# Kernel optimization log

Measured on AMD Instinct MI355X. Metric: run time of the kernel, lower is better.

The kernel has to match this reference:

```python
import jax, jax.numpy as jnp
import numpy as np
import math

B, L, DP, DB, H, DH = 1, 256, 128, 128, 8, 32


def _ln(x, g, b, eps=1e-5):
    m = x.mean(-1, keepdims=True)
    v = x.var(-1, keepdims=True)
    return (x - m) / jnp.sqrt(v + eps) * g + b


def setup_inputs() -> dict:
    key = jax.random.key(0)
    ks = jax.random.split(key, 12)
    s_in = 1.0 / math.sqrt(DP)
    s_hd = 1.0 / math.sqrt(H * DH)
    return {
        "pair": jax.random.normal(ks[0], (B, L, L, DP), jnp.float32),
        "bias": jax.random.normal(ks[1], (B, L, L, DB), jnp.float32),
        "mask": jax.random.randint(ks[2], (B, L), 0, 2, jnp.int32),
        "g_pair": jnp.ones((DP,), jnp.float32),
        "b_pair": jnp.zeros((DP,), jnp.float32),
        "g_bias": jnp.ones((DB,), jnp.float32),
        "b_bias": jnp.zeros((DB,), jnp.float32),
        "Wq": jax.random.normal(ks[3], (DP, H * DH), jnp.float32) * s_in,
        "Wk": jax.random.normal(ks[4], (DP, H * DH), jnp.float32) * s_in,
        "Wv": jax.random.normal(ks[5], (DP, H * DH), jnp.float32) * s_in,
        "Wb": jax.random.normal(ks[6], (DB, H), jnp.float32) * s_in,
        "Wg": jax.random.normal(ks[7], (DP, H * DH), jnp.float32) * s_in,
        "bg": jnp.ones((H * DH,), jnp.float32),
        "Wo": jax.random.normal(ks[8], (H * DH, DP), jnp.float32) * s_hd,
        "bo": jnp.zeros((DP,), jnp.float32),
    }


def reference(pair, bias, mask, g_pair, b_pair, g_bias, b_bias,
              Wq, Wk, Wv, Wb, Wg, bg, Wo, bo):
    is_row = True
    scaling = 1.0 / math.sqrt(DH)

    mask_b = (mask == 0)                               # [B,L], True = masked
    mask_2d = mask_b[:, None, :] | mask_b[:, :, None]  # [B,L,L]

    p = jnp.nan_to_num(pair)
    bi = jnp.nan_to_num(bias)
    if is_row:
        p = p.transpose(0, 2, 1, 3)
        bi = bi.transpose(0, 2, 1, 3)
        mask_2d = mask_2d.transpose(0, 2, 1)

    pn = _ln(p, g_pair, b_pair)        # [B,L,L,DP]
    bn = _ln(bi, g_bias, b_bias)       # [B,L,L,DB]

    q = (pn @ Wq).reshape(B, L, L, H, DH) * scaling
    k = (pn @ Wk).reshape(B, L, L, H, DH) / math.sqrt(L)
    v = (pn @ Wv).reshape(B, L, L, H, DH)
    b_proj = bn @ Wb                   # [B,L,L,H]
    gate = jax.nn.sigmoid(pn @ Wg + bg)  # [B,L,L,H*DH]

    # scores summed over the axial (n) axis AND head dim k
    attn = jnp.einsum('bnihk,bnjhk->bijh', q, k) + b_proj
    attn = jnp.where(mask_2d[..., None], -1e9, attn)
    attn = jax.nn.softmax(attn, axis=-2)  # over j

    out = jnp.einsum('bijh,bkjhd->bikhd', attn, v).reshape(B, L, L, H * DH)
    out = gate * out
    out = out @ Wo + bo                # [B,L,L,DP]
    if is_row:
        out = out.transpose(0, 2, 1, 3)
    # note: faithful to source — output mask uses the (permuted) mask_2d frame
    out = jnp.where(mask_2d[..., None], 0.0, out)
    return out
```

## Files before the change

### kernel.cpp

```cpp
#include <hip/hip_runtime.h>
#include <math.h>


typedef unsigned short u16;
typedef __attribute__((ext_vector_type(8))) short short8;
typedef __attribute__((ext_vector_type(4))) float float4v;

__device__ __forceinline__ u16 f2bf(float f) {
  unsigned int u = __float_as_uint(f);
  u += 0x7FFFu + ((u >> 16) & 1u);
  return (u16)(u >> 16);
}
__device__ __forceinline__ float bf2f(u16 h) {
  return __uint_as_float(((unsigned int)h) << 16);
}

__global__ __launch_bounds__(256) void k_ln(const float* __restrict__ x,
                                            const float* __restrict__ g,
                                            const float* __restrict__ b,
                                            u16* __restrict__ y) {
  int p = blockIdx.x * 4 + (threadIdx.x >> 6);
  int lane = threadIdx.x & 63;
  float2 xv = *(const float2*)(x + (size_t)p * 128 + lane * 2);
  float x0 = xv.x, x1 = xv.y;
  float s = x0 + x1, ss = x0 * x0 + x1 * x1;
#pragma unroll
  for (int off = 32; off; off >>= 1) {
    s += __shfl_xor(s, off);
    ss += __shfl_xor(ss, off);
  }
  float m = s * (1.0f / 128.0f);
  float v = ss * (1.0f / 128.0f) - m * m;
  float inv = rsqrtf(v + 1e-5f);
  float2 gv = *(const float2*)(g + lane * 2);
  float2 bv = *(const float2*)(b + lane * 2);
  float y0 = (x0 - m) * inv * gv.x + bv.x;
  float y1 = (x1 - m) * inv * gv.y + bv.y;
  unsigned int pk = (unsigned int)f2bf(y0) | ((unsigned int)f2bf(y1) << 16);
  *(unsigned int*)(y + (size_t)p * 128 + lane * 2) = pk;
}

__global__ __launch_bounds__(256) void k_lnbias_bproj(const float* __restrict__ x,
                                                      const float* __restrict__ g,
                                                      const float* __restrict__ b,
                                                      const float* __restrict__ Wb,
                                                      float* __restrict__ Bp) {
  const int t = threadIdx.x;
  const int row = t >> 3, h = t & 7;
  const int p = blockIdx.x * 32 + row;
  const int r = p >> 8, sc = p & 255;
  const float* rp = x + (size_t)p * 128 + h * 16;
  float4 xv[4];
#pragma unroll
  for (int i = 0; i < 4; ++i) xv[i] = ((const float4*)rp)[i];
  float s = 0.f, ss = 0.f;
#pragma unroll
  for (int i = 0; i < 4; ++i) {
    s += (xv[i].x + xv[i].y) + (xv[i].z + xv[i].w);
    ss += (xv[i].x * xv[i].x + xv[i].y * xv[i].y) + (xv[i].z * xv[i].z + xv[i].w * xv[i].w);
  }
#pragma unroll
  for (int off = 1; off <= 4; off <<= 1) {
    s += __shfl_xor(s, off);
    ss += __shfl_xor(ss, off);
  }
  float m = s * (1.0f / 128.0f);
  float var = ss * (1.0f / 128.0f) - m * m;
  float inv = rsqrtf(var + 1e-5f);
  float part[8];
#pragma unroll
  for (int hh = 0; hh < 8; ++hh) part[hh] = 0.f;
  const float4* g4 = (const float4*)(g + h * 16);
  const float4* b4 = (const float4*)(b + h * 16);
#pragma unroll
  for (int i4 = 0; i4 < 4; ++i4) {
    float4 gv = g4[i4], bv = b4[i4];
    float xs[4] = {xv[i4].x, xv[i4].y, xv[i4].z, xv[i4].w};
    float gs[4] = {gv.x, gv.y, gv.z, gv.w};
    float bs[4] = {bv.x, bv.y, bv.z, bv.w};
#pragma unroll
    for (int q = 0; q < 4; ++q) {
      int k = h * 16 + i4 * 4 + q;
      float xn = (xs[q] - m) * inv * gs[q] + bs[q];
      float4 w0 = *(const float4*)(Wb + k * 8);
      float4 w1 = *(const float4*)(Wb + k * 8 + 4);
      part[0] += xn * w0.x;
      part[1] += xn * w0.y;
      part[2] += xn * w0.z;
      part[3] += xn * w0.w;
      part[4] += xn * w1.x;
      part[5] += xn * w1.y;
      part[6] += xn * w1.z;
      part[7] += xn * w1.w;
    }
  }
#pragma unroll
  for (int off = 1; off <= 4; off <<= 1) {
#pragma unroll
    for (int hh = 0; hh < 8; ++hh) part[hh] += __shfl_xor(part[hh], off);
  }
  float val = (h == 0) ? part[0]
            : (h == 1) ? part[1]
            : (h == 2) ? part[2]
            : (h == 3) ? part[3]
            : (h == 4) ? part[4]
            : (h == 5) ? part[5]
            : (h == 6) ? part[6]
                       : part[7];
  Bp[(size_t)h * 65536 + (size_t)sc * 256 + r] = val;
}

__global__ __launch_bounds__(256) void k_wcvt(const float* __restrict__ Wq,
                                              const float* __restrict__ Wk,
                                              const float* __restrict__ Wv,
                                              const float* __restrict__ Wg,
                                              const float* __restrict__ Wo,
                                              u16* __restrict__ Wtb,
                                              u16* __restrict__ Wotb) {
  int idx = blockIdx.x * 256 + threadIdx.x;
  if (idx < 131072) {
    int w = idx >> 15, r = idx & 32767;
    int n = r >> 7, k = r & 127;
    const float* W = (w == 0) ? Wq : (w == 1) ? Wk : (w == 2) ? Wv : Wg;
    Wtb[(size_t)w * 32768 + n * 128 + k] = f2bf(W[k * 256 + n]);
  } else {
    int r = idx - 131072;
    int c = r >> 8, e = r & 255;
    Wotb[c * 256 + e] = f2bf(Wo[e * 128 + c]);
  }
}

__global__ __launch_bounds__(256) void k_proj_qkg(const u16* __restrict__ PNb,
                                                  const u16* __restrict__ Wtb,
                                                  const float* __restrict__ bg,
                                                  u16* __restrict__ Qr,
                                                  u16* __restrict__ Kr,
                                                  u16* __restrict__ Gb) {
  __shared__ u16 sb[128 * 72];
  const int t = threadIdx.x;
  const int wid = t >> 6, lane = t & 63;
  const int mrow = lane & 15, quad = lane >> 4;
  const int stripe = blockIdx.x;
  const int n0 = blockIdx.y * 64;
  const int wsel3 = blockIdx.z;
  const int wsel = (wsel3 == 2) ? 3 : wsel3;
  const u16* Wt = Wtb + (size_t)wsel * 32768;

  short8 bfr[4][4];
#pragma unroll
  for (int nt = 0; nt < 4; ++nt)
#pragma unroll
    for (int kk = 0; kk < 4; ++kk)
      bfr[nt][kk] = *(const short8*)(Wt + (size_t)(n0 + nt * 16 + mrow) * 128 + kk * 32 + quad * 8);

  float bgv[4];
#pragma unroll
  for (int nt = 0; nt < 4; ++nt) bgv[nt] = bg[n0 + nt * 16 + mrow];

  for (int it = 0; it < 4; ++it) {
    const int pb = stripe * 512 + it * 128;
    const int pw = pb + wid * 32;
    short8 afr[2][4];
#pragma unroll
    for (int mt = 0; mt < 2; ++mt)
#pragma unroll
      for (int kk = 0; kk < 4; ++kk)
        afr[mt][kk] =
            *(const short8*)(PNb + (size_t)(pw + mt * 16 + mrow) * 128 + kk * 32 + quad * 8);
    float4v acc[2][4];
#pragma unroll
    for (int mt = 0; mt < 2; ++mt)
#pragma unroll
      for (int nt = 0; nt < 4; ++nt) acc[mt][nt] = (float4v){0.f, 0.f, 0.f, 0.f};
#pragma unroll
    for (int kk = 0; kk < 4; ++kk)
#pragma unroll
      for (int mt = 0; mt < 2; ++mt)
#pragma unroll
        for (int nt = 0; nt < 4; ++nt)
          acc[mt][nt] = __builtin_amdgcn_mfma_f32_16x16x32_bf16(afr[mt][kk], bfr[nt][kk],
                                                                acc[mt][nt], 0, 0, 0);
#pragma unroll
    for (int mt = 0; mt < 2; ++mt)
#pragma unroll
      for (int nt = 0; nt < 4; ++nt)
#pragma unroll
        for (int reg = 0; reg < 4; ++reg) {
          float v = acc[mt][nt][reg];
          if (wsel3 == 0) v *= 0.17677669529663687f;
          else if (wsel3 == 1) v *= 0.0625f;
          else v = 1.f / (1.f + expf(-(v + bgv[nt])));
          sb[(wid * 32 + mt * 16 + quad * 4 + reg) * 72 + nt * 16 + mrow] = f2bf(v);
        }
    __syncthreads();
#pragma unroll
    for (int u4 = 0; u4 < 4; ++u4) {
      int u = u4 * 256 + t;
      int row = u >> 3, c8 = (u & 7) * 8;
      short8 vv = *(const short8*)&sb[row * 72 + c8];
      int p = pb + row;
      if (wsel3 == 0) {
        *(short8*)(Qr + (size_t)p * 256 + n0 + c8) = vv;
      } else if (wsel3 == 1) {
        *(short8*)(Kr + (size_t)p * 256 + n0 + c8) = vv;
      } else {
        int r = p >> 8, sc = p & 255;
        *(short8*)(Gb + ((size_t)sc * 256 + r) * 256 + n0 + c8) = vv;
      }
    }
    __syncthreads();
  }
}

__global__ __launch_bounds__(256) void k_projv(const u16* __restrict__ PNb,
                                               const u16* __restrict__ Wtb,
                                               u16* __restrict__ Vtb) {
  __shared__ u16 sb[128 * 136];
  const int t = threadIdx.x;
  const int wid = t >> 6, lane = t & 63;
  const int mrow = lane & 15, quad = lane >> 4;
  const int sc = blockIdx.x >> 1;
  const int r0 = (blockIdx.x & 1) * 128;
  short8 afr[2][4];
#pragma unroll
  for (int mt = 0; mt < 2; ++mt) {
    const int p = (r0 + wid * 32 + mt * 16 + mrow) * 256 + sc;
    const u16* ar = PNb + (size_t)p * 128 + quad * 8;
#pragma unroll
    for (int kk = 0; kk < 4; ++kk) afr[mt][kk] = *(const short8*)(ar + kk * 32);
  }
  const u16* Wt = Wtb + (size_t)2 * 32768;
  for (int half = 0; half < 2; ++half) {
#pragma unroll
    for (int nt8 = 0; nt8 < 8; ++nt8) {
      const int nt = half * 8 + nt8;
      float4v acc[2];
      acc[0] = (float4v){0.f, 0.f, 0.f, 0.f};
      acc[1] = (float4v){0.f, 0.f, 0.f, 0.f};
      const u16* br = Wt + (size_t)(nt * 16 + mrow) * 128 + quad * 8;
#pragma unroll
      for (int kk = 0; kk < 4; ++kk) {
        short8 bfr = *(const short8*)(br + kk * 32);
#pragma unroll
        for (int mt = 0; mt < 2; ++mt)
          acc[mt] = __builtin_amdgcn_mfma_f32_16x16x32_bf16(afr[mt][kk], bfr, acc[mt], 0, 0, 0);
      }
#pragma unroll
      for (int mt = 0; mt < 2; ++mt)
#pragma unroll
        for (int reg = 0; reg < 4; ++reg)
          sb[(wid * 32 + mt * 16 + quad * 4 + reg) * 136 + nt8 * 16 + mrow] =
              f2bf(acc[mt][reg]);
    }
    __syncthreads();
#pragma unroll
    for (int it = 0; it < 8; ++it) {
      int u = it * 256 + t;
      int c = u & 127, rg = u >> 7;
      short8 vv;
#pragma unroll
      for (int q = 0; q < 8; ++q) vv[q] = (short)sb[(rg * 8 + q) * 136 + c];
      int n = half * 128 + c;
      int h = n >> 5, d = n & 31;
      *(short8*)(Vtb + (size_t)h * 2097152 + (size_t)(sc * 32 + d) * 256 + r0 + rg * 8) = vv;
    }
    __syncthreads();
  }
}

__global__ __launch_bounds__(256) void k_logits_mfma(const u16* __restrict__ Qr,
                                                     const u16* __restrict__ Kr,
                                                     float* __restrict__ Lg2) {
  __shared__ u16 Qs[128 * 40];
  __shared__ u16 Ks[128 * 40];
  const int t = threadIdx.x;
  const int wid = t >> 6, lane = t & 63;
  const int mrow = lane & 15, quad = lane >> 4;
  const int i0 = (blockIdx.x >> 1) * 128, j0 = (blockIdx.x & 1) * 128;
  const int h = blockIdx.y;
  const int wi = wid >> 1, wj = wid & 1;
  float4v acc[4][4];
#pragma unroll
  for (int a = 0; a < 4; ++a)
#pragma unroll
    for (int bq = 0; bq < 4; ++bq) acc[a][bq] = (float4v){0.f, 0.f, 0.f, 0.f};

  for (int ck = 0; ck < 32; ++ck) {
    const int sc = blockIdx.z * 32 + ck;
    __syncthreads();
#pragma unroll
    for (int u = 0; u < 2; ++u) {
      int id = u * 256 + t;
      int rr = id >> 2, c8 = (id & 3) * 8;
      *(short8*)&Qs[rr * 40 + c8] =
          *(const short8*)(Qr + ((size_t)((i0 + rr) * 256 + sc)) * 256 + h * 32 + c8);
      *(short8*)&Ks[rr * 40 + c8] =
          *(const short8*)(Kr + ((size_t)((j0 + rr) * 256 + sc)) * 256 + h * 32 + c8);
    }
    __syncthreads();
    short8 afr[4], bfr[4];
#pragma unroll
    for (int mt = 0; mt < 4; ++mt)
      afr[mt] = *(const short8*)&Qs[(wi * 64 + mt * 16 + mrow) * 40 + quad * 8];
#pragma unroll
    for (int nn = 0; nn < 4; ++nn)
      bfr[nn] = *(const short8*)&Ks[(wj * 64 + nn * 16 + mrow) * 40 + quad * 8];
#pragma unroll
    for (int mt = 0; mt < 4; ++mt)
#pragma unroll
      for (int nn = 0; nn < 4; ++nn)
        acc[mt][nn] = __builtin_amdgcn_mfma_f32_16x16x32_bf16(afr[mt], bfr[nn], acc[mt][nn], 0, 0, 0);
  }
  float* slab = Lg2 + ((size_t)blockIdx.z * 8 + h) * 65536;
#pragma unroll
  for (int mt = 0; mt < 4; ++mt)
#pragma unroll
    for (int nn = 0; nn < 4; ++nn) {
      int j = j0 + wj * 64 + nn * 16 + mrow;
#pragma unroll
      for (int reg = 0; reg < 4; ++reg) {
        int i = i0 + wi * 64 + mt * 16 + quad * 4 + reg;
        slab[(size_t)i * 256 + j] = acc[mt][nn][reg];
      }
    }
}

__global__ __launch_bounds__(256) void k_softmax(const float* __restrict__ Bp,
                                                 const float* __restrict__ Lg2,
                                                 const int* __restrict__ mask,
                                                 u16* __restrict__ Ab) {
  const int i = blockIdx.x, h = blockIdx.y;
  const int j = threadIdx.x;
  __shared__ float red[4], red2[4];
  const size_t off = (size_t)h * 65536 + (size_t)i * 256 + j;
  float x = Bp[off];
#pragma unroll
  for (int z = 0; z < 8; ++z) x += Lg2[(size_t)z * 524288 + off];
  bool mi = (mask[i] == 0);
  if (mi || (mask[j] == 0)) x = -1e9f;
  float mx = x;
#pragma unroll
  for (int off2 = 32; off2; off2 >>= 1) mx = fmaxf(mx, __shfl_xor(mx, off2));
  int wave = j >> 6;
  if ((j & 63) == 0) red[wave] = mx;
  __syncthreads();
  mx = fmaxf(fmaxf(red[0], red[1]), fmaxf(red[2], red[3]));
  float e = expf(x - mx);
  float sm = e;
#pragma unroll
  for (int off2 = 32; off2; off2 >>= 1) sm += __shfl_xor(sm, off2);
  if ((j & 63) == 0) red2[wave] = sm;
  __syncthreads();
  sm = red2[0] + red2[1] + red2[2] + red2[3];
  Ab[off] = f2bf(e / sm);
}

__global__ __launch_bounds__(256) void k_av_mfma(const u16* __restrict__ Ab,
                                                 const u16* __restrict__ Vtb,
                                                 const u16* __restrict__ Gb,
                                                 u16* __restrict__ GOb) {
  __shared__ u16 As[64 * 264];
  const int t = threadIdx.x;
  const int wid = t >> 6, lane = t & 63;
  const int mrow = lane & 15, quad = lane >> 4;
  const int h = blockIdx.z;
  const int i0 = blockIdx.y * 64;
  const u16* ag = Ab + (size_t)h * 65536 + (size_t)i0 * 256;
#pragma unroll
  for (int u = 0; u < 8; ++u) {
    int id = u * 256 + t;
    int rr = id >> 5, c8 = (id & 31) * 8;
    *(short8*)&As[rr * 264 + c8] = *(const short8*)(ag + (size_t)rr * 256 + c8);
  }
  __syncthreads();
  const u16* vg = Vtb + (size_t)h * 2097152;
  for (int nt4 = 0; nt4 < 4; ++nt4) {
    const int nbase = blockIdx.x * 1024 + wid * 256 + nt4 * 64;
    float4v acc[4][4];
#pragma unroll
    for (int a = 0; a < 4; ++a)
#pragma unroll
      for (int bq = 0; bq < 4; ++bq) acc[a][bq] = (float4v){0.f, 0.f, 0.f, 0.f};
#pragma unroll
    for (int kk = 0; kk < 8; ++kk) {
      short8 afr[4], bfr[4];
#pragma unroll
      for (int mt = 0; mt < 4; ++mt)
        afr[mt] = *(const short8*)&As[(mt * 16 + mrow) * 264 + kk * 32 + quad * 8];
#pragma unroll
      for (int nn = 0; nn < 4; ++nn)
        bfr[nn] = *(const short8*)(vg + (size_t)(nbase + nn * 16 + mrow) * 256 + kk * 32 + quad * 8);
#pragma unroll
      for (int mt = 0; mt < 4; ++mt)
#pragma unroll
        for (int nn = 0; nn < 4; ++nn)
          acc[mt][nn] = __builtin_amdgcn_mfma_f32_16x16x32_bf16(afr[mt], bfr[nn], acc[mt][nn], 0, 0, 0);
    }
#pragma unroll
    for (int mt = 0; mt < 4; ++mt)
#pragma unroll
      for (int nn = 0; nn < 4; ++nn) {
        int n = nbase + nn * 16 + mrow;
        int kslot = n >> 5, d = n & 31;
        int e = h * 32 + d;
#pragma unroll
        for (int reg = 0; reg < 4; ++reg) {
          int i = i0 + mt * 16 + quad * 4 + reg;
          size_t idx = ((size_t)i * 256 + kslot) * 256 + e;
          float gv = bf2f(Gb[idx]);
          GOb[idx] = f2bf(acc[mt][nn][reg] * gv);
        }
      }
  }
}

__global__ __launch_bounds__(256) void k_out_mfma(const u16* __restrict__ GOb,
                                                  const u16* __restrict__ Wotb,
                                                  const float* __restrict__ bo,
                                                  const int* __restrict__ mask,
                                                  float* __restrict__ out) {
  const int wid = threadIdx.x >> 6, lane = threadIdx.x & 63;
  const int mrow = lane & 15, quad = lane >> 4;
  const int m0 = blockIdx.x * 128 + wid * 32;
  short8 afr[2][8];
#pragma unroll
  for (int mt = 0; mt < 2; ++mt) {
    const u16* ar = GOb + (size_t)(m0 + mt * 16 + mrow) * 256 + quad * 8;
#pragma unroll
    for (int kk = 0; kk < 8; ++kk) afr[mt][kk] = *(const short8*)(ar + kk * 32);
  }
  for (int nt = 0; nt < 8; ++nt) {
    float4v acc[2];
    acc[0] = (float4v){0.f, 0.f, 0.f, 0.f};
    acc[1] = (float4v){0.f, 0.f, 0.f, 0.f};
    const u16* br = Wotb + (size_t)(nt * 16 + mrow) * 256 + quad * 8;
#pragma unroll
    for (int kk = 0; kk < 8; ++kk) {
      short8 bfr = *(const short8*)(br + kk * 32);
#pragma unroll
      for (int mt = 0; mt < 2; ++mt)
        acc[mt] = __builtin_amdgcn_mfma_f32_16x16x32_bf16(afr[mt][kk], bfr, acc[mt], 0, 0, 0);
    }
    const int c = nt * 16 + mrow;
    float bov = bo[c];
#pragma unroll
    for (int mt = 0; mt < 2; ++mt) {
#pragma unroll
      for (int reg = 0; reg < 4; ++reg) {
        int m = m0 + mt * 16 + quad * 4 + reg;
        int i = m >> 8, kq = m & 255;
        float v = acc[mt][reg] + bov;
        bool z = (mask[i] == 0) || (mask[kq] == 0);
        out[((size_t)kq * 256 + i) * 128 + c] = z ? 0.f : v;
      }
    }
  }
}

extern "C" void kernel_launch(void* const* d_in, const int* in_sizes, int n_in,
                              void* d_out, int out_size, void* d_ws, size_t ws_size,
                              hipStream_t stream) {
  const float* pair = (const float*)d_in[0];
  const float* bias = (const float*)d_in[1];
  const int* mask = (const int*)d_in[2];
  const float* g_pair = (const float*)d_in[3];
  const float* b_pair = (const float*)d_in[4];
  const float* g_bias = (const float*)d_in[5];
  const float* b_bias = (const float*)d_in[6];
  const float* Wq = (const float*)d_in[7];
  const float* Wk = (const float*)d_in[8];
  const float* Wv = (const float*)d_in[9];
  const float* Wb = (const float*)d_in[10];
  const float* Wg = (const float*)d_in[11];
  const float* bg = (const float*)d_in[12];
  const float* Wo = (const float*)d_in[13];
  const float* bo = (const float*)d_in[14];
  float* out = (float*)d_out;
  char* ws = (char*)d_ws;

  u16* PNb = (u16*)(ws + 0);
  u16* Qr = (u16*)(ws + 16777216);
  u16* Kr = (u16*)(ws + 50331648);
  u16* Vtb = (u16*)(ws + 83886080);
  u16* Gb = (u16*)(ws + 117440512);
  u16* GOb = (u16*)(ws + 150994944);
  float* Bp = (float*)(ws + 184549376);
  u16* Ab = (u16*)(ws + 186646528);
  u16* Wtb = (u16*)(ws + 187695104);
  u16* Wotb = (u16*)(ws + 187957248);
  float* Lg2 = (float*)(ws + 188022784);

  k_ln<<<16384, 256, 0, stream>>>(pair, g_pair, b_pair, PNb);
  k_wcvt<<<640, 256, 0, stream>>>(Wq, Wk, Wv, Wg, Wo, Wtb, Wotb);
  k_lnbias_bproj<<<2048, 256, 0, stream>>>(bias, g_bias, b_bias, Wb, Bp);
  k_proj_qkg<<<dim3(128, 4, 3), 256, 0, stream>>>(PNb, Wtb, bg, Qr, Kr, Gb);
  k_projv<<<512, 256, 0, stream>>>(PNb, Wtb, Vtb);
  k_logits_mfma<<<dim3(4, 8, 8), 256, 0, stream>>>(Qr, Kr, Lg2);
  k_softmax<<<dim3(256, 8), 256, 0, stream>>>(Bp, Lg2, mask, Ab);
  k_av_mfma<<<dim3(8, 4, 8), 256, 0, stream>>>(Ab, Vtb, Gb, GOb);
  k_out_mfma<<<512, 256, 0, stream>>>(GOb, Wotb, bo, mask, out);
}
```

Baseline: 361.8 us.

## Store Q/K/G in quad-packed layout and widen logits split-K

The Q, K and gate projections now write MFMA accumulator results straight to global memory in a layout that packs four consecutive rows per element column. This drops the shared-memory staging pass and its two barriers per iteration. The logits kernel reads this layout, covering 4 sc slots per group with a 64-wide k chunk, and its split-K grid doubles to 16 z-slices. The softmax therefore sums 16 partial slabs instead of 8, which costs more Lg2 traffic and partial-sum writes. The AV kernel loads the gate as one 4-element vector instead of 4 scalar loads.

```diff
diff --git a/kernel.cpp b/kernel.cpp
--- a/kernel.cpp
+++ b/kernel.cpp
@@ -4,6 +4,7 @@
 
 typedef unsigned short u16;
 typedef __attribute__((ext_vector_type(8))) short short8;
+typedef __attribute__((ext_vector_type(4))) short short4v;
 typedef __attribute__((ext_vector_type(4))) float float4v;
 
 __device__ __forceinline__ u16 f2bf(float f) {
@@ -133,10 +134,9 @@
 __global__ __launch_bounds__(256) void k_proj_qkg(const u16* __restrict__ PNb,
                                                   const u16* __restrict__ Wtb,
                                                   const float* __restrict__ bg,
-                                                  u16* __restrict__ Qr,
-                                                  u16* __restrict__ Kr,
-                                                  u16* __restrict__ Gb) {
-  __shared__ u16 sb[128 * 72];
+                                                  u16* __restrict__ Qr4,
+                                                  u16* __restrict__ Kr4,
+                                                  u16* __restrict__ G2) {
   const int t = threadIdx.x;
   const int wid = t >> 6, lane = t & 63;
   const int mrow = lane & 15, quad = lane >> 4;
@@ -145,6 +145,7 @@
   const int wsel3 = blockIdx.z;
   const int wsel = (wsel3 == 2) ? 3 : wsel3;
   const u16* Wt = Wtb + (size_t)wsel * 32768;
+  u16* dst = (wsel3 == 0) ? Qr4 : (wsel3 == 1) ? Kr4 : G2;
 
   short8 bfr[4][4];
 #pragma unroll
@@ -158,8 +159,7 @@
   for (int nt = 0; nt < 4; ++nt) bgv[nt] = bg[n0 + nt * 16 + mrow];
 
   for (int it = 0; it < 4; ++it) {
-    const int pb = stripe * 512 + it * 128;
-    const int pw = pb + wid * 32;
+    const int pw = stripe * 512 + it * 128 + wid * 32;
     short8 afr[2][4];
 #pragma unroll
     for (int mt = 0; mt < 2; ++mt)
@@ -181,34 +181,23 @@
           acc[mt][nt] = __builtin_amdgcn_mfma_f32_16x16x32_bf16(afr[mt][kk], bfr[nt][kk],
                                                                 acc[mt][nt], 0, 0, 0);
 #pragma unroll
-    for (int mt = 0; mt < 2; ++mt)
-#pragma unroll
-      for (int nt = 0; nt < 4; ++nt)
+    for (int mt = 0; mt < 2; ++mt) {
+      const int prow4 = ((pw + mt * 16) >> 2) + quad;
+#pragma unroll
+      for (int nt = 0; nt < 4; ++nt) {
+        const int n = n0 + nt * 16 + mrow;
+        short4v pk;
 #pragma unroll
         for (int reg = 0; reg < 4; ++reg) {
           float v = acc[mt][nt][reg];
           if (wsel3 == 0) v *= 0.17677669529663687f;
           else if (wsel3 == 1) v *= 0.0625f;
           else v = 1.f / (1.f + expf(-(v + bgv[nt])));
-          sb[(wid * 32 + mt * 16 + quad * 4 + reg) * 72 + nt * 16 + mrow] = f2bf(v);
+          pk[reg] = (short)f2bf(v);
         }
-    __syncthreads();
-#pragma unroll
-    for (int u4 = 0; u4 < 4; ++u4) {
-      int u = u4 * 256 + t;
-      int row = u >> 3, c8 = (u & 7) * 8;
-      short8 vv = *(const short8*)&sb[row * 72 + c8];
-      int p = pb + row;
-      if (wsel3 == 0) {
-        *(short8*)(Qr + (size_t)p * 256 + n0 + c8) = vv;
-      } else if (wsel3 == 1) {
-        *(short8*)(Kr + (size_t)p * 256 + n0 + c8) = vv;
-      } else {
-        int r = p >> 8, sc = p & 255;
-        *(short8*)(Gb + ((size_t)sc * 256 + r) * 256 + n0 + c8) = vv;
-      }
-    }
-    __syncthreads();
+        *(short4v*)(dst + ((size_t)prow4 * 256 + n) * 4) = pk;
+      }
+    }
   }
 }
 
@@ -268,16 +257,17 @@
   }
 }
 
-__global__ __launch_bounds__(256) void k_logits_mfma(const u16* __restrict__ Qr,
-                                                     const u16* __restrict__ Kr,
+__global__ __launch_bounds__(256) void k_logits_mfma(const u16* __restrict__ Qr4,
+                                                     const u16* __restrict__ Kr4,
                                                      float* __restrict__ Lg2) {
-  __shared__ u16 Qs[128 * 40];
-  __shared__ u16 Ks[128 * 40];
+  __shared__ u16 Qs[128 * 72];
+  __shared__ u16 Ks[128 * 72];
   const int t = threadIdx.x;
   const int wid = t >> 6, lane = t & 63;
   const int mrow = lane & 15, quad = lane >> 4;
   const int i0 = (blockIdx.x >> 1) * 128, j0 = (blockIdx.x & 1) * 128;
   const int h = blockIdx.y;
+  const int z = blockIdx.z;
   const int wi = wid >> 1, wj = wid & 1;
   float4v acc[4][4];
 #pragma unroll
@@ -285,33 +275,39 @@
 #pragma unroll
     for (int bq = 0; bq < 4; ++bq) acc[a][bq] = (float4v){0.f, 0.f, 0.f, 0.f};
 
-  for (int ck = 0; ck < 32; ++ck) {
-    const int sc = blockIdx.z * 32 + ck;
-    __syncthreads();
-#pragma unroll
-    for (int u = 0; u < 2; ++u) {
-      int id = u * 256 + t;
-      int rr = id >> 2, c8 = (id & 3) * 8;
-      *(short8*)&Qs[rr * 40 + c8] =
-          *(const short8*)(Qr + ((size_t)((i0 + rr) * 256 + sc)) * 256 + h * 32 + c8);
-      *(short8*)&Ks[rr * 40 + c8] =
-          *(const short8*)(Kr + ((size_t)((j0 + rr) * 256 + sc)) * 256 + h * 32 + c8);
-    }
-    __syncthreads();
-    short8 afr[4], bfr[4];
-#pragma unroll
-    for (int mt = 0; mt < 4; ++mt)
-      afr[mt] = *(const short8*)&Qs[(wi * 64 + mt * 16 + mrow) * 40 + quad * 8];
-#pragma unroll
-    for (int nn = 0; nn < 4; ++nn)
-      bfr[nn] = *(const short8*)&Ks[(wj * 64 + nn * 16 + mrow) * 40 + quad * 8];
-#pragma unroll
-    for (int mt = 0; mt < 4; ++mt)
-#pragma unroll
-      for (int nn = 0; nn < 4; ++nn)
-        acc[mt][nn] = __builtin_amdgcn_mfma_f32_16x16x32_bf16(afr[mt], bfr[nn], acc[mt][nn], 0, 0, 0);
-  }
-  float* slab = Lg2 + ((size_t)blockIdx.z * 8 + h) * 65536;
+  for (int g = 0; g < 4; ++g) {
+    const int sc4 = z * 4 + g;
+    for (int sub = 0; sub < 2; ++sub) {
+      __syncthreads();
+#pragma unroll
+      for (int itq = 0; itq < 4; ++itq) {
+        int u = itq * 256 + t;
+        int i_loc = u >> 3, c16 = sub * 8 + (u & 7);
+        size_t qoff = ((size_t)((i0 + i_loc) * 64 + sc4) * 256 + h * 32 + c16 * 2) * 4;
+        *(short8*)&Qs[i_loc * 72 + (u & 7) * 8] = *(const short8*)(Qr4 + qoff);
+        size_t koff = ((size_t)((j0 + i_loc) * 64 + sc4) * 256 + h * 32 + c16 * 2) * 4;
+        *(short8*)&Ks[i_loc * 72 + (u & 7) * 8] = *(const short8*)(Kr4 + koff);
+      }
+      __syncthreads();
+#pragma unroll
+      for (int kk = 0; kk < 2; ++kk) {
+        short8 afr[4], bfr[4];
+#pragma unroll
+        for (int mt = 0; mt < 4; ++mt)
+          afr[mt] = *(const short8*)&Qs[(wi * 64 + mt * 16 + mrow) * 72 + kk * 32 + quad * 8];
+#pragma unroll
+        for (int nn = 0; nn < 4; ++nn)
+          bfr[nn] = *(const short8*)&Ks[(wj * 64 + nn * 16 + mrow) * 72 + kk * 32 + quad * 8];
+#pragma unroll
+        for (int mt = 0; mt < 4; ++mt)
+#pragma unroll
+          for (int nn = 0; nn < 4; ++nn)
+            acc[mt][nn] =
+                __builtin_amdgcn_mfma_f32_16x16x32_bf16(afr[mt], bfr[nn], acc[mt][nn], 0, 0, 0);
+      }
+    }
+  }
+  float* slab = Lg2 + ((size_t)z * 8 + h) * 65536;
 #pragma unroll
   for (int mt = 0; mt < 4; ++mt)
 #pragma unroll
@@ -335,7 +331,7 @@
   const size_t off = (size_t)h * 65536 + (size_t)i * 256 + j;
   float x = Bp[off];
 #pragma unroll
-  for (int z = 0; z < 8; ++z) x += Lg2[(size_t)z * 524288 + off];
+  for (int z = 0; z < 16; ++z) x += Lg2[(size_t)z * 524288 + off];
   bool mi = (mask[i] == 0);
   if (mi || (mask[j] == 0)) x = -1e9f;
   float mx = x;
@@ -357,7 +353,7 @@
 
 __global__ __launch_bounds__(256) void k_av_mfma(const u16* __restrict__ Ab,
                                                  const u16* __restrict__ Vtb,
-                                                 const u16* __restrict__ Gb,
+                                                 const u16* __restrict__ G2,
                                                  u16* __restrict__ GOb) {
   __shared__ u16 As[64 * 264];
   const int t = threadIdx.x;
@@ -400,14 +396,16 @@
     for (int mt = 0; mt < 4; ++mt)
 #pragma unroll
       for (int nn = 0; nn < 4; ++nn) {
-        int n = nbase + nn * 16 + mrow;
-        int kslot = n >> 5, d = n & 31;
-        int e = h * 32 + d;
+        const int kslot = (nbase + nn * 16) >> 5;
+        const int d = (nn & 1) * 16 + mrow;
+        const int e = h * 32 + d;
+        const int p4 = kslot * 64 + ((i0 + mt * 16) >> 2) + quad;
+        short4v g4 = *(const short4v*)(G2 + ((size_t)p4 * 256 + e) * 4);
 #pragma unroll
         for (int reg = 0; reg < 4; ++reg) {
           int i = i0 + mt * 16 + quad * 4 + reg;
           size_t idx = ((size_t)i * 256 + kslot) * 256 + e;
-          float gv = bf2f(Gb[idx]);
+          float gv = bf2f((u16)g4[reg]);
           GOb[idx] = f2bf(acc[mt][nn][reg] * gv);
         }
       }
@@ -479,10 +477,10 @@
   char* ws = (char*)d_ws;
 
   u16* PNb = (u16*)(ws + 0);
-  u16* Qr = (u16*)(ws + 16777216);
-  u16* Kr = (u16*)(ws + 50331648);
+  u16* Qr4 = (u16*)(ws + 16777216);
+  u16* Kr4 = (u16*)(ws + 50331648);
   u16* Vtb = (u16*)(ws + 83886080);
-  u16* Gb = (u16*)(ws + 117440512);
+  u16* G2 = (u16*)(ws + 117440512);
   u16* GOb = (u16*)(ws + 150994944);
   float* Bp = (float*)(ws + 184549376);
   u16* Ab = (u16*)(ws + 186646528);
@@ -493,10 +491,10 @@
   k_ln<<<16384, 256, 0, stream>>>(pair, g_pair, b_pair, PNb);
   k_wcvt<<<640, 256, 0, stream>>>(Wq, Wk, Wv, Wg, Wo, Wtb, Wotb);
   k_lnbias_bproj<<<2048, 256, 0, stream>>>(bias, g_bias, b_bias, Wb, Bp);
-  k_proj_qkg<<<dim3(128, 4, 3), 256, 0, stream>>>(PNb, Wtb, bg, Qr, Kr, Gb);
+  k_proj_qkg<<<dim3(128, 4, 3), 256, 0, stream>>>(PNb, Wtb, bg, Qr4, Kr4, G2);
   k_projv<<<512, 256, 0, stream>>>(PNb, Wtb, Vtb);
-  k_logits_mfma<<<dim3(4, 8, 8), 256, 0, stream>>>(Qr, Kr, Lg2);
+  k_logits_mfma<<<dim3(4, 8, 16), 256, 0, stream>>>(Qr4, Kr4, Lg2);
   k_softmax<<<dim3(256, 8), 256, 0, stream>>>(Bp, Lg2, mask, Ab);
-  k_av_mfma<<<dim3(8, 4, 8), 256, 0, stream>>>(Ab, Vtb, Gb, GOb);
+  k_av_mfma<<<dim3(8, 4, 8), 256, 0, stream>>>(Ab, Vtb, G2, GOb);
   k_out_mfma<<<512, 256, 0, stream>>>(GOb, Wotb, bo, mask, out);
 }
```

After: 338.2 us. 1.07x faster.
